# Kernel optimization log

Hardware: AMD Instinct MI355X
Metric: run time of the kernel (lower is better)

Reference implementation:

```python
import jax, jax.numpy as jnp
import numpy as np

D_MODEL, D_STATE, N_HEADS = 1024, 64, 16


def setup_inputs() -> dict:
    key = jax.random.key(0)
    ks = jax.random.split(key, 4)
    B, T = 4, 4096
    s = 1.0 / np.sqrt(D_MODEL)
    x = jax.random.normal(ks[0], (B, T, D_MODEL), dtype=jnp.float32)
    h_prev = jnp.zeros((B, N_HEADS, D_STATE), dtype=jnp.float32)
    gate_w = jax.random.normal(ks[1], (2 * N_HEADS * D_STATE, D_MODEL), dtype=jnp.float32) * s
    # torch init: forget-gate bias = 1, input-gate bias = 0
    gate_b = jnp.concatenate([jnp.ones(N_HEADS * D_STATE), jnp.zeros(N_HEADS * D_STATE)]).astype(jnp.float32)
    value_w = jax.random.normal(ks[2], (N_HEADS * D_STATE, D_MODEL), dtype=jnp.float32) * s
    out_w = jax.random.normal(ks[3], (D_MODEL, N_HEADS * D_STATE), dtype=jnp.float32) * s
    return {"x": x, "h_prev": h_prev, "gate_w": gate_w, "gate_b": gate_b, "value_w": value_w, "out_w": out_w}


def reference(x, h_prev, gate_w, gate_b, value_w, out_w):
    B, T, _ = x.shape
    H, S = N_HEADS, D_STATE
    gates = (jnp.einsum('btd,gd->btg', x, gate_w) + gate_b).reshape(B, T, 2, H, S)
    A = jax.nn.sigmoid(gates[:, :, 0])   # [B,T,H,S] forget gate
    Bg = jax.nn.sigmoid(gates[:, :, 1])  # [B,T,H,S] input gate
    V = jnp.einsum('btd,vd->btv', x, value_w).reshape(B, T, H, S)

    def step(h, inp):
        a_t, bv_t = inp
        h = a_t * h + bv_t
        return h, h

    # time-major for scan; precompute B*V elementwise product
    a_tm = jnp.moveaxis(A, 1, 0)                # [T,B,H,S]
    bv_tm = jnp.moveaxis(Bg * V, 1, 0)          # [T,B,H,S]
    h_last, h_seq = jax.lax.scan(step, h_prev, (a_tm, bv_tm))
    h_flat = jnp.moveaxis(h_seq, 0, 1).reshape(B, T, H * S)
    y = jnp.einsum('btv,dv->btd', h_flat, out_w)  # dropout is identity at p=0/eval
    return y, h_last
```

## Files before the change

kernel.cpp:

```cpp
#include <hip/hip_runtime.h>
#include <cstdint>
#include <cstddef>


typedef _Float16 f16;
typedef _Float16 f16x2 __attribute__((ext_vector_type(2)));
typedef _Float16 f16x8 __attribute__((ext_vector_type(8)));
typedef float    f32x4 __attribute__((ext_vector_type(4)));

__device__ __forceinline__ void gload_lds16(const void* g, void* l) {
  __builtin_amdgcn_global_load_lds(
      (const __attribute__((address_space(1))) void*)g,
      (__attribute__((address_space(3))) void*)l, 16, 0, 0);
}

__device__ __forceinline__ float sigmoidf_(float x) {
  return 1.0f / (1.0f + __expf(-x));
}

__global__ __launch_bounds__(256) void cast_f32_to_f16(
    const float* __restrict__ src, f16* __restrict__ dst, int n8) {
  int i = blockIdx.x * 256 + threadIdx.x;
  if (i >= n8) return;
  const float4* s4 = (const float4*)src;
  float4 v0 = s4[2 * i], v1 = s4[2 * i + 1];
  f16x8 o;
  o[0] = (f16)v0.x; o[1] = (f16)v0.y; o[2] = (f16)v0.z; o[3] = (f16)v0.w;
  o[4] = (f16)v1.x; o[5] = (f16)v1.y; o[6] = (f16)v1.z; o[7] = (f16)v1.w;
  *(f16x8*)(dst + (size_t)i * 8) = o;
}

template <int EPI>
__global__ __launch_bounds__(256, 3) void gemm_bt(
    const f16* __restrict__ A, const f16* __restrict__ Bw,
    const float* __restrict__ gate_b,
    void* __restrict__ o0v, void* __restrict__ o1v, void* __restrict__ o2v) {
  constexpr int K = 1024;
  __shared__ __align__(16) f16 As[128 * 64];
  __shared__ __align__(16) f16 Bs[128 * 64];
  const int tid  = threadIdx.x;
  const int lane = tid & 63;
  const int quad = lane >> 4;
  const int wv   = tid >> 6;
  const int wrow = wv & 1, wcol = wv >> 1;
  const int n0 = blockIdx.y * 128;
  const int m0 = blockIdx.x * 128;

  const f16* ga[4];
  const f16* gb[4];
  f16* la[4];
  f16* lb[4];
#pragma unroll
  for (int j = 0; j < 4; ++j) {
    int s   = j * 256 + tid;
    int row = s >> 3;
    int kc  = (s & 7) ^ (row & 7);
    ga[j] = A  + (size_t)(n0 + row) * K + kc * 8;
    gb[j] = Bw + (size_t)(m0 + row) * K + kc * 8;
    la[j] = &As[s * 8];
    lb[j] = &Bs[s * 8];
  }

  f32x4 acc[4][4];
#pragma unroll
  for (int mi = 0; mi < 4; ++mi)
#pragma unroll
    for (int ni = 0; ni < 4; ++ni) acc[mi][ni] = (f32x4){0.f, 0.f, 0.f, 0.f};

  for (int k0 = 0; k0 < K; k0 += 64) {
#pragma unroll
    for (int j = 0; j < 4; ++j) gload_lds16(ga[j], la[j]);
#pragma unroll
    for (int j = 0; j < 4; ++j) gload_lds16(gb[j], lb[j]);
#pragma unroll
    for (int j = 0; j < 4; ++j) { ga[j] += 64; gb[j] += 64; }
    __syncthreads();
#pragma unroll
    for (int kk = 0; kk < 2; ++kk) {
      f16x8 af[4], bfv[4];
#pragma unroll
      for (int mi = 0; mi < 4; ++mi) {
        int row  = wrow * 64 + mi * 16 + (lane & 15);
        int slot = row * 8 + ((kk * 4 + quad) ^ (row & 7));
        af[mi] = *(const f16x8*)(&As[slot * 8]);
      }
#pragma unroll
      for (int ni = 0; ni < 4; ++ni) {
        int row  = wcol * 64 + ni * 16 + (lane & 15);
        int slot = row * 8 + ((kk * 4 + quad) ^ (row & 7));
        bfv[ni] = *(const f16x8*)(&Bs[slot * 8]);
      }
#pragma unroll
      for (int mi = 0; mi < 4; ++mi)
#pragma unroll
        for (int ni = 0; ni < 4; ++ni)
          acc[mi][ni] = __builtin_amdgcn_mfma_f32_16x16x32_f16(
              af[mi], bfv[ni], acc[mi][ni], 0, 0, 0);
    }
    __syncthreads();
  }

#pragma unroll
  for (int mi = 0; mi < 4; ++mi) {
#pragma unroll
    for (int ni = 0; ni < 4; ++ni) {
      const int m = m0 + wcol * 64 + ni * 16 + (lane & 15);
#pragma unroll
      for (int r = 0; r < 4; ++r) {
        const int n = n0 + wrow * 64 + mi * 16 + quad * 4 + r;
        float val = acc[mi][ni][r];
        if (EPI == 0) {
          if (m < 2048) {
            f16 sv = (f16)sigmoidf_(val + gate_b[m]);
            if (m < 1024)
              ((f16*)o0v)[(size_t)n * 1024 + m] = sv;
            else
              ((f16*)o1v)[(size_t)n * 1024 + (m - 1024)] = sv;
          } else {
            ((f16*)o2v)[(size_t)n * 1024 + (m - 2048)] = (f16)val;
          }
        } else {
          ((float*)o0v)[(size_t)n * 1024 + m] = val;
        }
      }
    }
  }
}

__global__ __launch_bounds__(256) void scan_pass1(
    const f16x2* __restrict__ a, const f16x2* __restrict__ bg,
    const f16x2* __restrict__ v, float2* __restrict__ Ac,
    float2* __restrict__ Uc) {
  const int c2 = blockIdx.x * 256 + threadIdx.x;
  const int j = blockIdx.y;
  const int b = blockIdx.z;
  const size_t base = ((size_t)(b * 4096 + j * 128)) * 512 + c2;
  float P0 = 1.f, P1 = 1.f, U0 = 0.f, U1 = 0.f;
#pragma unroll 4
  for (int t = 0; t < 128; ++t) {
    const size_t o = base + (size_t)t * 512;
    f16x2 at = a[o], gt = bg[o], vt = v[o];
    float a0 = (float)at[0], a1 = (float)at[1];
    float bv0 = (float)gt[0] * (float)vt[0];
    float bv1 = (float)gt[1] * (float)vt[1];
    P0 *= a0; P1 *= a1;
    U0 = a0 * U0 + bv0;
    U1 = a1 * U1 + bv1;
  }
  const size_t o = ((size_t)(b * 32 + j)) * 512 + c2;
  Ac[o] = make_float2(P0, P1);
  Uc[o] = make_float2(U0, U1);
}

__global__ __launch_bounds__(256) void scan_pass2(
    const float* __restrict__ Ac, const float* __restrict__ Uc,
    const float* __restrict__ h_prev, float* __restrict__ Hs,
    float* __restrict__ hlast) {
  const int id = blockIdx.x * 256 + threadIdx.x;
  const int b = id >> 10, c = id & 1023;
  float H = h_prev[b * 1024 + c];
  for (int j = 0; j < 32; ++j) {
    const size_t o = ((size_t)(b * 32 + j)) * 1024 + c;
    Hs[o] = H;
    H = Ac[o] * H + Uc[o];
  }
  hlast[b * 1024 + c] = H;
}

__global__ __launch_bounds__(256) void scan_pass3(
    const f16x2* __restrict__ a, const f16x2* __restrict__ bg,
    const f16x2* __restrict__ v, const float2* __restrict__ Hs,
    f16x2* __restrict__ hb) {
  const int c2 = blockIdx.x * 256 + threadIdx.x;
  const int j = blockIdx.y;
  const int b = blockIdx.z;
  const size_t base = ((size_t)(b * 4096 + j * 128)) * 512 + c2;
  float2 H = Hs[((size_t)(b * 32 + j)) * 512 + c2];
  float h0 = H.x, h1 = H.y;
#pragma unroll 4
  for (int t = 0; t < 128; ++t) {
    const size_t o = base + (size_t)t * 512;
    f16x2 at = a[o], gt = bg[o], vt = v[o];
    float a0 = (float)at[0], a1 = (float)at[1];
    h0 = a0 * h0 + (float)gt[0] * (float)vt[0];
    h1 = a1 * h1 + (float)gt[1] * (float)vt[1];
    f16x2 hv; hv[0] = (f16)h0; hv[1] = (f16)h1;
    hb[o] = hv;
  }
}

extern "C" void kernel_launch(void* const* d_in, const int* in_sizes, int n_in,
                              void* d_out, int out_size, void* d_ws,
                              size_t ws_size, hipStream_t stream) {
  const float* x       = (const float*)d_in[0];
  const float* h_prev  = (const float*)d_in[1];
  const float* gate_w  = (const float*)d_in[2];
  const float* gate_b  = (const float*)d_in[3];
  const float* value_w = (const float*)d_in[4];
  const float* out_w   = (const float*)d_in[5];
  float* out = (float*)d_out;

  char* ws = (char*)d_ws;
  f16*   xh   = (f16*)(ws);
  f16*   wgv  = (f16*)(ws + 33554432);
  f16*   owb  = (f16*)(ws + 39845888);
  f16*   abuf = (f16*)(ws + 41943040);
  f16*   g1   = (f16*)(ws + 75497472);
  f16*   vbuf = (f16*)(ws + 109051904);
  float* Ac   = (float*)(ws + 142606336);
  float* Uc   = (float*)(ws + 143130624);
  float* Hs   = (float*)(ws + 143654912);
  float* hlast = out + 16777216;

  cast_f32_to_f16<<<8192, 256, 0, stream>>>(x, xh, 2097152);
  cast_f32_to_f16<<<1024, 256, 0, stream>>>(gate_w, wgv, 262144);
  cast_f32_to_f16<<<512, 256, 0, stream>>>(value_w, wgv + 2048 * 1024, 131072);
  cast_f32_to_f16<<<512, 256, 0, stream>>>(out_w, owb, 131072);

  gemm_bt<0><<<dim3(24, 128), 256, 0, stream>>>(xh, wgv, gate_b, abuf, g1,
                                                vbuf);

  scan_pass1<<<dim3(2, 32, 4), 256, 0, stream>>>(
      (const f16x2*)abuf, (const f16x2*)g1, (const f16x2*)vbuf, (float2*)Ac,
      (float2*)Uc);
  scan_pass2<<<16, 256, 0, stream>>>(Ac, Uc, h_prev, Hs, hlast);
  scan_pass3<<<dim3(2, 32, 4), 256, 0, stream>>>(
      (const f16x2*)abuf, (const f16x2*)g1, (const f16x2*)vbuf,
      (const float2*)Hs, (f16x2*)xh);

  gemm_bt<1><<<dim3(8, 128), 256, 0, stream>>>(xh, owb, nullptr, out, nullptr,
                                               nullptr);
}
```

Baseline: 377.3 us.

## Fuse gate·value product into GEMM epilogue via interleaved weights and LDS-staged stores

```diff
diff --git a/kernel.cpp b/kernel.cpp
--- a/kernel.cpp
+++ b/kernel.cpp
@@ -18,26 +18,52 @@
   return 1.0f / (1.0f + __expf(-x));
 }
 
-__global__ __launch_bounds__(256) void cast_f32_to_f16(
-    const float* __restrict__ src, f16* __restrict__ dst, int n8) {
-  int i = blockIdx.x * 256 + threadIdx.x;
-  if (i >= n8) return;
-  const float4* s4 = (const float4*)src;
-  float4 v0 = s4[2 * i], v1 = s4[2 * i + 1];
+__global__ __launch_bounds__(256) void cast_pack(
+    const float* __restrict__ x, const float* __restrict__ gw,
+    const float* __restrict__ vw, const float* __restrict__ ow,
+    f16* __restrict__ xh, f16* __restrict__ wgv, f16* __restrict__ owb) {
+  const int XG = 2097152, GG = 262144, VG = 131072, OG = 131072;
+  int id = blockIdx.x * 256 + threadIdx.x;
+  const float* src;
+  f16* dst;
+  if (id < XG) {
+    src = x + (size_t)id * 8;
+    dst = xh + (size_t)id * 8;
+  } else if (id < XG + GG) {
+    int g = id - XG;
+    int row = g >> 7, col = g & 127;
+    int drow = (row < 1024) ? row : (1024 + 2 * (row - 1024));
+    src = gw + ((size_t)row << 10) + col * 8;
+    dst = wgv + ((size_t)drow << 10) + col * 8;
+  } else if (id < XG + GG + VG) {
+    int g = id - XG - GG;
+    int row = g >> 7, col = g & 127;
+    int drow = 1024 + 2 * row + 1;
+    src = vw + ((size_t)row << 10) + col * 8;
+    dst = wgv + ((size_t)drow << 10) + col * 8;
+  } else if (id < XG + GG + VG + OG) {
+    int g = id - XG - GG - VG;
+    src = ow + (size_t)g * 8;
+    dst = owb + (size_t)g * 8;
+  } else {
+    return;
+  }
+  float4 v0 = ((const float4*)src)[0], v1 = ((const float4*)src)[1];
   f16x8 o;
   o[0] = (f16)v0.x; o[1] = (f16)v0.y; o[2] = (f16)v0.z; o[3] = (f16)v0.w;
   o[4] = (f16)v1.x; o[5] = (f16)v1.y; o[6] = (f16)v1.z; o[7] = (f16)v1.w;
-  *(f16x8*)(dst + (size_t)i * 8) = o;
+  *(f16x8*)dst = o;
 }
 
 template <int EPI>
 __global__ __launch_bounds__(256, 3) void gemm_bt(
     const f16* __restrict__ A, const f16* __restrict__ Bw,
     const float* __restrict__ gate_b,
-    void* __restrict__ o0v, void* __restrict__ o1v, void* __restrict__ o2v) {
+    void* __restrict__ o0v, void* __restrict__ o1v) {
   constexpr int K = 1024;
-  __shared__ __align__(16) f16 As[128 * 64];
-  __shared__ __align__(16) f16 Bs[128 * 64];
+  __shared__ __align__(16) f16 S[17920];
+  f16* As = S;
+  f16* Bs = S + 8192;
   const int tid  = threadIdx.x;
   const int lane = tid & 63;
   const int quad = lane >> 4;
@@ -100,54 +126,91 @@
     __syncthreads();
   }
 
-#pragma unroll
-  for (int mi = 0; mi < 4; ++mi) {
-#pragma unroll
-    for (int ni = 0; ni < 4; ++ni) {
-      const int m = m0 + wcol * 64 + ni * 16 + (lane & 15);
-#pragma unroll
-      for (int r = 0; r < 4; ++r) {
-        const int n = n0 + wrow * 64 + mi * 16 + quad * 4 + r;
-        float val = acc[mi][ni][r];
-        if (EPI == 0) {
-          if (m < 2048) {
-            f16 sv = (f16)sigmoidf_(val + gate_b[m]);
-            if (m < 1024)
-              ((f16*)o0v)[(size_t)n * 1024 + m] = sv;
-            else
-              ((f16*)o1v)[(size_t)n * 1024 + (m - 1024)] = sv;
-          } else {
-            ((f16*)o2v)[(size_t)n * 1024 + (m - 2048)] = (f16)val;
+  if (EPI == 1) {
+#pragma unroll
+    for (int mi = 0; mi < 4; ++mi)
+#pragma unroll
+      for (int ni = 0; ni < 4; ++ni) {
+        const int m = m0 + wcol * 64 + ni * 16 + (lane & 15);
+#pragma unroll
+        for (int r = 0; r < 4; ++r) {
+          const int n = n0 + wrow * 64 + mi * 16 + quad * 4 + r;
+          ((float*)o0v)[(size_t)n * 1024 + m] = acc[mi][ni][r];
+        }
+      }
+    return;
+  }
+
+  if (m0 < 1024) {
+#pragma unroll
+    for (int mi = 0; mi < 4; ++mi)
+#pragma unroll
+      for (int ni = 0; ni < 4; ++ni) {
+        const int ml = wcol * 64 + ni * 16 + (lane & 15);
+#pragma unroll
+        for (int r = 0; r < 4; ++r) {
+          const int nl = wrow * 64 + mi * 16 + quad * 4 + r;
+          S[nl * 136 + ml] = (f16)sigmoidf_(acc[mi][ni][r] + gate_b[m0 + ml]);
+        }
+      }
+    __syncthreads();
+    f16* o0 = (f16*)o0v;
+#pragma unroll
+    for (int i = 0; i < 8; ++i) {
+      int ch = i * 256 + tid;
+      int row = ch >> 4, cc = ch & 15;
+      f16x8 vv = *(const f16x8*)&S[row * 136 + cc * 8];
+      *(f16x8*)(o0 + (size_t)(n0 + row) * 1024 + m0 + cc * 8) = vv;
+    }
+  } else {
+    const int c0 = (m0 - 1024) >> 1;
+#pragma unroll
+    for (int mi = 0; mi < 4; ++mi)
+#pragma unroll
+      for (int ni = 0; ni < 4; ++ni) {
+        const int ml = wcol * 64 + ni * 16 + (lane & 15);
+#pragma unroll
+        for (int r = 0; r < 4; ++r) {
+          float val = acc[mi][ni][r];
+          float pv = __shfl_xor(val, 1, 64);
+          if (!(lane & 1)) {
+            const int c = ml >> 1;
+            const int nl = wrow * 64 + mi * 16 + quad * 4 + r;
+            S[nl * 72 + c] =
+                (f16)(sigmoidf_(val + gate_b[1024 + c0 + c]) * pv);
           }
-        } else {
-          ((float*)o0v)[(size_t)n * 1024 + m] = val;
         }
       }
+    __syncthreads();
+    f16* o1 = (f16*)o1v;
+#pragma unroll
+    for (int i = 0; i < 4; ++i) {
+      int ch = i * 256 + tid;
+      int row = ch >> 3, cc = ch & 7;
+      f16x8 vv = *(const f16x8*)&S[row * 72 + cc * 8];
+      *(f16x8*)(o1 + (size_t)(n0 + row) * 1024 + c0 + cc * 8) = vv;
     }
   }
 }
 
 __global__ __launch_bounds__(256) void scan_pass1(
-    const f16x2* __restrict__ a, const f16x2* __restrict__ bg,
-    const f16x2* __restrict__ v, float2* __restrict__ Ac,
-    float2* __restrict__ Uc) {
+    const f16x2* __restrict__ a, const f16x2* __restrict__ bv,
+    float2* __restrict__ Ac, float2* __restrict__ Uc) {
   const int c2 = blockIdx.x * 256 + threadIdx.x;
   const int j = blockIdx.y;
   const int b = blockIdx.z;
-  const size_t base = ((size_t)(b * 4096 + j * 128)) * 512 + c2;
+  const size_t base = ((size_t)(b * 4096 + j * 32)) * 512 + c2;
   float P0 = 1.f, P1 = 1.f, U0 = 0.f, U1 = 0.f;
-#pragma unroll 4
-  for (int t = 0; t < 128; ++t) {
+#pragma unroll 8
+  for (int t = 0; t < 32; ++t) {
     const size_t o = base + (size_t)t * 512;
-    f16x2 at = a[o], gt = bg[o], vt = v[o];
+    f16x2 at = a[o], bt = bv[o];
     float a0 = (float)at[0], a1 = (float)at[1];
-    float bv0 = (float)gt[0] * (float)vt[0];
-    float bv1 = (float)gt[1] * (float)vt[1];
     P0 *= a0; P1 *= a1;
-    U0 = a0 * U0 + bv0;
-    U1 = a1 * U1 + bv1;
-  }
-  const size_t o = ((size_t)(b * 32 + j)) * 512 + c2;
+    U0 = a0 * U0 + (float)bt[0];
+    U1 = a1 * U1 + (float)bt[1];
+  }
+  const size_t o = ((size_t)(b * 128 + j)) * 512 + c2;
   Ac[o] = make_float2(P0, P1);
   Uc[o] = make_float2(U0, U1);
 }
@@ -159,8 +222,8 @@
   const int id = blockIdx.x * 256 + threadIdx.x;
   const int b = id >> 10, c = id & 1023;
   float H = h_prev[b * 1024 + c];
-  for (int j = 0; j < 32; ++j) {
-    const size_t o = ((size_t)(b * 32 + j)) * 1024 + c;
+  for (int j = 0; j < 128; ++j) {
+    const size_t o = ((size_t)(b * 128 + j)) * 1024 + c;
     Hs[o] = H;
     H = Ac[o] * H + Uc[o];
   }
@@ -168,22 +231,20 @@
 }
 
 __global__ __launch_bounds__(256) void scan_pass3(
-    const f16x2* __restrict__ a, const f16x2* __restrict__ bg,
-    const f16x2* __restrict__ v, const float2* __restrict__ Hs,
-    f16x2* __restrict__ hb) {
+    const f16x2* __restrict__ a, const f16x2* __restrict__ bv,
+    const float2* __restrict__ Hs, f16x2* __restrict__ hb) {
   const int c2 = blockIdx.x * 256 + threadIdx.x;
   const int j = blockIdx.y;
   const int b = blockIdx.z;
-  const size_t base = ((size_t)(b * 4096 + j * 128)) * 512 + c2;
-  float2 H = Hs[((size_t)(b * 32 + j)) * 512 + c2];
+  const size_t base = ((size_t)(b * 4096 + j * 32)) * 512 + c2;
+  float2 H = Hs[((size_t)(b * 128 + j)) * 512 + c2];
   float h0 = H.x, h1 = H.y;
-#pragma unroll 4
-  for (int t = 0; t < 128; ++t) {
+#pragma unroll 8
+  for (int t = 0; t < 32; ++t) {
     const size_t o = base + (size_t)t * 512;
-    f16x2 at = a[o], gt = bg[o], vt = v[o];
-    float a0 = (float)at[0], a1 = (float)at[1];
-    h0 = a0 * h0 + (float)gt[0] * (float)vt[0];
-    h1 = a1 * h1 + (float)gt[1] * (float)vt[1];
+    f16x2 at = a[o], bt = bv[o];
+    h0 = (float)at[0] * h0 + (float)bt[0];
+    h1 = (float)at[1] * h1 + (float)bt[1];
     f16x2 hv; hv[0] = (f16)h0; hv[1] = (f16)h1;
     hb[o] = hv;
   }
@@ -205,29 +266,22 @@
   f16*   wgv  = (f16*)(ws + 33554432);
   f16*   owb  = (f16*)(ws + 39845888);
   f16*   abuf = (f16*)(ws + 41943040);
-  f16*   g1   = (f16*)(ws + 75497472);
-  f16*   vbuf = (f16*)(ws + 109051904);
-  float* Ac   = (float*)(ws + 142606336);
-  float* Uc   = (float*)(ws + 143130624);
-  float* Hs   = (float*)(ws + 143654912);
+  f16*   bvb  = (f16*)(ws + 75497472);
+  float* Ac   = (float*)(ws + 109051904);
+  float* Uc   = (float*)(ws + 111149056);
+  float* Hs   = (float*)(ws + 113246208);
   float* hlast = out + 16777216;
 
-  cast_f32_to_f16<<<8192, 256, 0, stream>>>(x, xh, 2097152);
-  cast_f32_to_f16<<<1024, 256, 0, stream>>>(gate_w, wgv, 262144);
-  cast_f32_to_f16<<<512, 256, 0, stream>>>(value_w, wgv + 2048 * 1024, 131072);
-  cast_f32_to_f16<<<512, 256, 0, stream>>>(out_w, owb, 131072);
-
-  gemm_bt<0><<<dim3(24, 128), 256, 0, stream>>>(xh, wgv, gate_b, abuf, g1,
-                                                vbuf);
-
-  scan_pass1<<<dim3(2, 32, 4), 256, 0, stream>>>(
-      (const f16x2*)abuf, (const f16x2*)g1, (const f16x2*)vbuf, (float2*)Ac,
-      (float2*)Uc);
+  cast_pack<<<10240, 256, 0, stream>>>(x, gate_w, value_w, out_w, xh, wgv,
+                                       owb);
+
+  gemm_bt<0><<<dim3(24, 128), 256, 0, stream>>>(xh, wgv, gate_b, abuf, bvb);
+
+  scan_pass1<<<dim3(2, 128, 4), 256, 0, stream>>>(
+      (const f16x2*)abuf, (const f16x2*)bvb, (float2*)Ac, (float2*)Uc);
   scan_pass2<<<16, 256, 0, stream>>>(Ac, Uc, h_prev, Hs, hlast);
-  scan_pass3<<<dim3(2, 32, 4), 256, 0, stream>>>(
-      (const f16x2*)abuf, (const f16x2*)g1, (const f16x2*)vbuf,
-      (const float2*)Hs, (f16x2*)xh);
-
-  gemm_bt<1><<<dim3(8, 128), 256, 0, stream>>>(xh, owb, nullptr, out, nullptr,
-                                               nullptr);
-}
+  scan_pass3<<<dim3(2, 128, 4), 256, 0, stream>>>(
+      (const f16x2*)abuf, (const f16x2*)bvb, (const float2*)Hs, (f16x2*)xh);
+
+  gemm_bt<1><<<dim3(8, 128), 256, 0, stream>>>(xh, owb, nullptr, out, nullptr);
+}
```

New measurement: 373.3 us. No clear change (-1.0%).
